# Performance work log

Hardware: AMD Instinct MI355X
Metric: run time of the kernel (lower is better)

Reference implementation:

```python
import jax, jax.numpy as jnp
import numpy as np

VS = 0.4
SENT = np.int32(2_000_000_000)  # > max lin code (1000^3)
EPS = 1e-5


def setup_inputs() -> dict:
    key = jax.random.key(0)
    ks = jax.random.split(key, 16)
    B, N, Cin, Cout = 8, 65536, 16, 128
    xyz = jax.random.uniform(ks[0], (B, N, 3), jnp.float32) * 51.2  # 128^3 voxel grid @ 0.4m
    feat = jax.random.normal(ks[1], (B, N, Cin), jnp.float32)
    mask = (jax.random.uniform(ks[2], (B, N)) < 0.9).astype(jnp.float32)
    def conv_w(k, ci, co):
        return jax.random.normal(k, (27, ci, co), jnp.float32) * (1.0 / np.sqrt(27.0 * ci))
    return {
        'xyz': xyz, 'feat': feat, 'mask': mask,
        'W1': conv_w(ks[3], Cin, 32), 'b1': jnp.zeros((32,), jnp.float32),
        'g1': jnp.ones((32,), jnp.float32), 'be1': jnp.zeros((32,), jnp.float32),
        'W2': conv_w(ks[4], 32, 64), 'b2': jnp.zeros((64,), jnp.float32),
        'g2': jnp.ones((64,), jnp.float32), 'be2': jnp.zeros((64,), jnp.float32),
        'W3': conv_w(ks[5], 64, Cout), 'b3': jnp.zeros((Cout,), jnp.float32),
        'g3': jnp.ones((Cout,), jnp.float32), 'be3': jnp.zeros((Cout,), jnp.float32),
    }


def _voxelize(lin_b, f_b, m_b):
    # sort-based unique with inverse; fixed capacity N slots (sentinel-padded)
    N = lin_b.shape[0]
    order = jnp.argsort(lin_b)
    s = lin_b[order]
    isnew = jnp.concatenate([jnp.ones((1,), bool), s[1:] != s[:-1]])
    rank = (jnp.cumsum(isnew) - 1).astype(jnp.int32)
    inv = jnp.zeros_like(lin_b).at[order].set(rank)          # point -> voxel slot
    unq = jnp.full_like(lin_b, SENT).at[rank].set(s)         # sorted unique codes, sentinel fill
    fsum = jax.ops.segment_sum(f_b * m_b[:, None], inv, num_segments=N)
    cnt = jnp.clip(jax.ops.segment_sum(m_b, inv, num_segments=N), 1.0)
    return unq, inv, fsum / cnt[:, None]


def _subm_conv(vfeat, unq, valid, W, b):
    # submanifold 3x3x3 conv on active voxels; neighbor lookup via binary search in sorted codes
    B, N, _ = vfeat.shape
    x = unq % 1000
    y = (unq // 1000) % 1000
    z = unq // 1000000
    brow = jnp.arange(B)[:, None]
    out = jnp.zeros((B, N, W.shape[-1]), vfeat.dtype)
    for ko in range(27):
        dz, dy, dx = ko // 9 - 1, (ko // 3) % 3 - 1, ko % 3 - 1
        ncode = unq + dx + 1000 * dy + 1000000 * dz
        inb = ((x + dx >= 0) & (x + dx < 1000) & (y + dy >= 0) & (y + dy < 1000)
               & (z + dz >= 0) & (z + dz < 1000))
        idx = jnp.clip(jax.vmap(jnp.searchsorted)(unq, ncode), 0, N - 1)
        found = (jnp.take_along_axis(unq, idx, 1) == ncode) & inb & valid
        nf = vfeat[brow, idx] * found[..., None].astype(vfeat.dtype)
        out = out + nf @ W[ko]
    return (out + b) * valid[..., None].astype(vfeat.dtype)


def _bn_relu(xv, g, be, valid):
    # BatchNorm1d (training stats) over valid voxel rows only, then ReLU
    w = valid[..., None].astype(xv.dtype)
    n = jnp.maximum(w.sum(), 1.0)
    mean = (xv * w).sum((0, 1)) / n
    var = (((xv - mean) ** 2) * w).sum((0, 1)) / n
    yv = (xv - mean) * jax.lax.rsqrt(var + EPS) * g + be
    return jax.nn.relu(yv) * w


def reference(xyz, feat, mask, W1, b1, g1, be1, W2, b2, g2, be2, W3, b3, g3, be3):
    B, N, _ = feat.shape
    origin = xyz.reshape(-1, 3).min(0)
    v = jnp.clip(((xyz - origin) / VS).astype(jnp.int32), 0, None)   # [B,N,3]
    lin = v[..., 0] + 1000 * (v[..., 1] + 1000 * v[..., 2])          # [B,N]
    unq, inv, vfeat = jax.vmap(_voxelize)(lin, feat, mask)
    valid = unq < SENT
    h = _bn_relu(_subm_conv(vfeat, unq, valid, W1, b1), g1, be1, valid)
    h = _bn_relu(_subm_conv(h, unq, valid, W2, b2), g2, be2, valid)
    h = _bn_relu(_subm_conv(h, unq, valid, W3, b3), g3, be3, valid)
    # scatter voxel features back to points (exact match: inv maps point -> its voxel slot)
    out_f = h[jnp.arange(B)[:, None], inv]                           # [B,N,Cout]
    return out_f * mask[..., None]
```

## Files before the change

### kernel.cpp

```cpp
#include <hip/hip_runtime.h>

#define NPTS   65536
#define NBATCH 8
#define TSIZE  131072
#define TM1    (TSIZE - 1)
#define CAP    8192
#define PPB    64
#define BMW    65536
#define STG    64
#define PCS    16

__device__ __forceinline__ unsigned hashf(int code) {
    unsigned u = (unsigned)code * 2654435761u;
    return (u >> 13) & TM1;
}

__global__ void init_origin(int* ob) {
    if (threadIdx.x < 3) ob[threadIdx.x] = 0x7F800000;
}

__global__ void minred(const float* __restrict__ xyz, int* __restrict__ ob) {
    int tid = threadIdx.x;
    float mx = INFINITY, my = INFINITY, mz = INFINITY;
    size_t total = (size_t)NBATCH * NPTS;
    for (size_t i = (size_t)blockIdx.x * blockDim.x + tid; i < total;
         i += (size_t)gridDim.x * blockDim.x) {
        mx = fminf(mx, xyz[i * 3 + 0]);
        my = fminf(my, xyz[i * 3 + 1]);
        mz = fminf(mz, xyz[i * 3 + 2]);
    }
    __shared__ float sx[256], sy[256], sz[256];
    sx[tid] = mx; sy[tid] = my; sz[tid] = mz;
    __syncthreads();
    for (int s = 128; s > 0; s >>= 1) {
        if (tid < s) {
            sx[tid] = fminf(sx[tid], sx[tid + s]);
            sy[tid] = fminf(sy[tid], sy[tid + s]);
            sz[tid] = fminf(sz[tid], sz[tid + s]);
        }
        __syncthreads();
    }
    if (tid == 0) {
        atomicMin(&ob[0], __float_as_int(sx[0]));
        atomicMin(&ob[1], __float_as_int(sy[0]));
        atomicMin(&ob[2], __float_as_int(sz[0]));
    }
}

__global__ void build_codes(const float* __restrict__ xyz, const int* __restrict__ ob,
                            int* __restrict__ pslot, int* __restrict__ hashk,
                            int* __restrict__ scnt) {
    int b = blockIdx.y;
    int p = blockIdx.x * blockDim.x + threadIdx.x;
    size_t gi = (size_t)b * NPTS + p;
    float ox = __int_as_float(ob[0]);
    float oy = __int_as_float(ob[1]);
    float oz = __int_as_float(ob[2]);
    float x = xyz[gi * 3 + 0], y = xyz[gi * 3 + 1], z = xyz[gi * 3 + 2];
    int vx = (int)((x - ox) / 0.4f); if (vx < 0) vx = 0;
    int vy = (int)((y - oy) / 0.4f); if (vy < 0) vy = 0;
    int vz = (int)((z - oz) / 0.4f); if (vz < 0) vz = 0;
    int code = vx | (vy << 7) | (vz << 14);
    int* hk = hashk + (size_t)b * TSIZE;
    unsigned s = hashf(code);
    while (true) {
        int prev = atomicCAS(&hk[s], -1, code);
        if (prev == -1 || prev == code) break;
        s = (s + 1) & TM1;
    }
    pslot[gi] = (int)s;
    atomicAdd(&scnt[(size_t)b * TSIZE + s], 1);
}

__global__ void assign_ids(const int* __restrict__ hashk, int* __restrict__ hashv,
                           int* __restrict__ nvox, int* __restrict__ voxcode,
                           unsigned* __restrict__ bitmap, const int* __restrict__ scnt,
                           int* __restrict__ vnpts) {
    int b = blockIdx.y;
    int s = blockIdx.x * blockDim.x + threadIdx.x;
    int k = hashk[(size_t)b * TSIZE + s];
    if (k != -1) {
        int id = atomicAdd(&nvox[b], 1);
        hashv[(size_t)b * TSIZE + s] = id;
        voxcode[(size_t)b * NPTS + id] = k;
        vnpts[(size_t)b * NPTS + id] = scnt[(size_t)b * TSIZE + s];
        atomicOr(&bitmap[(size_t)b * BMW + (k >> 5)], 1u << (k & 31));
    }
}

__global__ void point_pass(const int* __restrict__ pslot, const int* __restrict__ scnt,
                           const int* __restrict__ hashv, const float* __restrict__ feat,
                           const float* __restrict__ mask, int* __restrict__ inv,
                           float* __restrict__ cntf, float* __restrict__ fsum) {
    int b = blockIdx.y;
    int p = blockIdx.x * blockDim.x + threadIdx.x;
    size_t gi = (size_t)b * NPTS + p;
    int s = pslot[gi];
    int v = hashv[(size_t)b * TSIZE + s];
    inv[gi] = v;
    int n = scnt[(size_t)b * TSIZE + s];
    float m = mask[gi];
    const float4* f4 = (const float4*)(feat + gi * 16);
    float4 f0 = f4[0], f1 = f4[1], f2 = f4[2], f3 = f4[3];
    float* fs = fsum + ((size_t)b * NPTS + v) * 16;
    if (n == 1) {
        float4 o0 = {f0.x * m, f0.y * m, f0.z * m, f0.w * m};
        float4 o1 = {f1.x * m, f1.y * m, f1.z * m, f1.w * m};
        float4 o2 = {f2.x * m, f2.y * m, f2.z * m, f2.w * m};
        float4 o3 = {f3.x * m, f3.y * m, f3.z * m, f3.w * m};
        float4* fs4 = (float4*)fs;
        fs4[0] = o0; fs4[1] = o1; fs4[2] = o2; fs4[3] = o3;
    } else {
        atomicAdd(&cntf[(size_t)b * NPTS + v], m);
        atomicAdd(&fs[0],  f0.x * m); atomicAdd(&fs[1],  f0.y * m);
        atomicAdd(&fs[2],  f0.z * m); atomicAdd(&fs[3],  f0.w * m);
        atomicAdd(&fs[4],  f1.x * m); atomicAdd(&fs[5],  f1.y * m);
        atomicAdd(&fs[6],  f1.z * m); atomicAdd(&fs[7],  f1.w * m);
        atomicAdd(&fs[8],  f2.x * m); atomicAdd(&fs[9],  f2.y * m);
        atomicAdd(&fs[10], f2.z * m); atomicAdd(&fs[11], f2.w * m);
        atomicAdd(&fs[12], f3.x * m); atomicAdd(&fs[13], f3.y * m);
        atomicAdd(&fs[14], f3.z * m); atomicAdd(&fs[15], f3.w * m);
    }
}

__global__ void vfeat_div(float* __restrict__ fsum, const float* __restrict__ cntf,
                          const int* __restrict__ vnpts, const int* __restrict__ nvox) {
    int b = blockIdx.y;
    int v = blockIdx.x * blockDim.x + threadIdx.x;
    if (v >= nvox[b]) return;
    if (vnpts[(size_t)b * NPTS + v] <= 1) return;
    float cn = fmaxf(cntf[(size_t)b * NPTS + v], 1.0f);
    float* fs = fsum + ((size_t)b * NPTS + v) * 16;
    #pragma unroll
    for (int c = 0; c < 16; c++) fs[c] /= cn;
}

__global__ __launch_bounds__(256) void build_pairs(
    const int* __restrict__ hashk, const int* __restrict__ hashv,
    const int* __restrict__ voxcode, const int* __restrict__ nvox,
    const unsigned* __restrict__ bitmap,
    unsigned* __restrict__ pairs, int* __restrict__ paircnt) {
    int b = blockIdx.y;
    int t = threadIdx.x;
    int v = blockIdx.x * 256 + t;
    __shared__ int lcnt[32];
    __shared__ int lbase[32];
    __shared__ unsigned s_pay[27 * STG];
    if (t < 32) lcnt[t] = 0;
    __syncthreads();

    bool active = (v < nvox[b]);
    int code = 0;
    if (active) code = voxcode[(size_t)b * NPTS + v];
    int x = code & 127, y = (code >> 7) & 127, z = code >> 14;
    const unsigned* bm = bitmap + (size_t)b * BMW;
    const int* hk = hashk + (size_t)b * TSIZE;
    const int* hv = hashv + (size_t)b * TSIZE;

    int ncode[13];
    unsigned hitmask = 0;
    #pragma unroll
    for (int d = 0; d < 13; d++) {
        int dz = d / 9 - 1, r9 = d % 9;
        int dy = r9 / 3 - 1, dx = r9 % 3 - 1;
        int nx = x + dx, ny = y + dy, nz = z + dz;
        bool inb = active && ((unsigned)nx <= 127u) && ((unsigned)ny <= 127u) &&
                   ((unsigned)nz <= 127u);
        int nc = nx | (ny << 7) | (nz << 14);
        ncode[d] = nc;
        unsigned w = 0;
        if (inb) w = bm[nc >> 5];
        if (inb && ((w >> (nc & 31)) & 1u)) hitmask |= 1u << d;
    }

    #pragma unroll
    for (int d = 0; d < 13; d++) {
        if (hitmask & (1u << d)) {
            int nc = ncode[d];
            unsigned s = hashf(nc);
            int nb = -1;
            while (true) {
                int k = hk[s];
                if (k == nc) { nb = hv[s]; break; }
                if (k == -1) break;
                s = (s + 1) & TM1;
            }
            if (nb >= 0) {
                unsigned p1 = ((unsigned)v << 16) | (unsigned)nb;
                unsigned p2 = ((unsigned)nb << 16) | (unsigned)v;
                int l1 = atomicAdd(&lcnt[d], 1);
                if (l1 < STG) {
                    s_pay[d * STG + l1] = p1;
                } else {
                    int gs = atomicAdd(&paircnt[(b * 27 + d) * PCS], 1);
                    if (gs < CAP) pairs[(size_t)(b * 27 + d) * CAP + gs] = p1;
                }
                int k2 = 26 - d;
                int l2 = atomicAdd(&lcnt[k2], 1);
                if (l2 < STG) {
                    s_pay[k2 * STG + l2] = p2;
                } else {
                    int gs = atomicAdd(&paircnt[(b * 27 + k2) * PCS], 1);
                    if (gs < CAP) pairs[(size_t)(b * 27 + k2) * CAP + gs] = p2;
                }
            }
        }
    }
    __syncthreads();

    if (t < 27) {
        int n = lcnt[t]; if (n > STG) n = STG;
        lbase[t] = (n > 0) ? atomicAdd(&paircnt[(b * 27 + t) * PCS], n) : 0;
    }
    __syncthreads();

    for (int k = t; k < 27 * STG; k += 256) {
        int bkt = k / STG, i = k % STG;
        int n = lcnt[bkt]; if (n > STG) n = STG;
        if (i < n) {
            int gs = lbase[bkt] + i;
            if (gs < CAP) pairs[(size_t)(b * 27 + bkt) * CAP + gs] = s_pay[k];
        }
    }
}

template <int Cin, int Cout, bool XFORM>
__global__ __launch_bounds__(256) void conv_center(
    const float* __restrict__ in, float* __restrict__ outp,
    const float* __restrict__ W13, const float* __restrict__ bias,
    const float* __restrict__ sc, const float* __restrict__ sh,
    const int* __restrict__ nvox) {
    constexpr int BR  = 64;
    constexpr int CT  = (Cout < 64) ? Cout : 64;
    constexpr int RG  = 256 / CT;
    constexpr int RPT = BR / RG;
    constexpr int J   = Cout / CT;
    int b = blockIdx.y;
    int nv = nvox[b];
    int v0 = blockIdx.x * BR;
    if (v0 >= nv) return;
    __shared__ __align__(16) float A_s[Cin][BR + 4];
    __shared__ __align__(16) float W_s[Cin * Cout];
    int t = threadIdx.x;
    for (int i4 = t; i4 < Cin * Cout / 4; i4 += 256)
        ((float4*)W_s)[i4] = ((const float4*)W13)[i4];
    const float* inb = in + (size_t)b * NPTS * Cin;
    for (int i4 = t; i4 < BR * Cin / 4; i4 += 256) {
        int lin = i4 * 4;
        int r = lin / Cin, ci = lin % Cin;
        float4 val = *(const float4*)&inb[(size_t)(v0 + r) * Cin + ci];
        if (XFORM) {
            val.x = fmaxf(val.x * sc[ci + 0] + sh[ci + 0], 0.0f);
            val.y = fmaxf(val.y * sc[ci + 1] + sh[ci + 1], 0.0f);
            val.z = fmaxf(val.z * sc[ci + 2] + sh[ci + 2], 0.0f);
            val.w = fmaxf(val.w * sc[ci + 3] + sh[ci + 3], 0.0f);
        }
        A_s[ci + 0][r] = val.x;
        A_s[ci + 1][r] = val.y;
        A_s[ci + 2][r] = val.z;
        A_s[ci + 3][r] = val.w;
    }
    __syncthreads();
    int c = t % CT;
    int r0 = (t / CT) * RPT;
    float acc[RPT][J];
    #pragma unroll
    for (int r = 0; r < RPT; r++)
        #pragma unroll
        for (int j = 0; j < J; j++) acc[r][j] = 0.0f;
    #pragma unroll 4
    for (int ci = 0; ci < Cin; ci++) {
        float4 a4[RPT / 4];
        #pragma unroll
        for (int k = 0; k < RPT / 4; k++)
            a4[k] = *(const float4*)&A_s[ci][r0 + 4 * k];
        float w[J];
        #pragma unroll
        for (int j = 0; j < J; j++) w[j] = W_s[ci * Cout + c + CT * j];
        #pragma unroll
        for (int k = 0; k < RPT / 4; k++) {
            #pragma unroll
            for (int j = 0; j < J; j++) {
                acc[4 * k + 0][j] += a4[k].x * w[j];
                acc[4 * k + 1][j] += a4[k].y * w[j];
                acc[4 * k + 2][j] += a4[k].z * w[j];
                acc[4 * k + 3][j] += a4[k].w * w[j];
            }
        }
    }
    float* ob = outp + (size_t)b * NPTS * Cout;
    #pragma unroll
    for (int r = 0; r < RPT; r++) {
        int row = v0 + r0 + r;
        if (row < nv) {
            #pragma unroll
            for (int j = 0; j < J; j++)
                ob[(size_t)row * Cout + c + CT * j] = acc[r][j] + bias[c + CT * j];
        }
    }
}

template <int Cin, int Cout, bool XFORM>
__global__ __launch_bounds__(256) void conv_off(
    const float* __restrict__ in, float* __restrict__ outp,
    const float* __restrict__ W, const float* __restrict__ sc,
    const float* __restrict__ sh, const unsigned* __restrict__ pairs,
    const int* __restrict__ paircnt) {
    constexpr int BR  = PPB;
    constexpr int CT  = (Cout < 64) ? Cout : 64;
    constexpr int RG  = 256 / CT;
    constexpr int RPT = BR / RG;
    constexpr int J   = Cout / CT;
    int bk = blockIdx.y;
    int ko = bk % 27;
    int b  = bk / 27;
    int cnt = paircnt[bk * PCS];
    if (cnt > CAP) cnt = CAP;
    int start = blockIdx.x * BR;
    if (start >= cnt) return;
    int nActive = cnt - start; if (nActive > BR) nActive = BR;
    __shared__ __align__(16) float A_s[Cin][BR + 4];
    __shared__ __align__(16) float W_s[Cin * Cout];
    __shared__ unsigned pr_s[BR];
    int t = threadIdx.x;
    const float* Wk = W + (size_t)ko * Cin * Cout;
    for (int i4 = t; i4 < Cin * Cout / 4; i4 += 256)
        ((float4*)W_s)[i4] = ((const float4*)Wk)[i4];
    const unsigned* pb = pairs + (size_t)bk * CAP + start;
    if (t < BR) pr_s[t] = pb[t];
    __syncthreads();
    const float* inb = in + (size_t)b * NPTS * Cin;
    for (int i4 = t; i4 < BR * Cin / 4; i4 += 256) {
        int lin = i4 * 4;
        int r = lin / Cin, ci = lin % Cin;
        int vin = (int)(pr_s[r] & 0xffffu);
        float4 val = *(const float4*)&inb[(size_t)vin * Cin + ci];
        if (XFORM) {
            val.x = fmaxf(val.x * sc[ci + 0] + sh[ci + 0], 0.0f);
            val.y = fmaxf(val.y * sc[ci + 1] + sh[ci + 1], 0.0f);
            val.z = fmaxf(val.z * sc[ci + 2] + sh[ci + 2], 0.0f);
            val.w = fmaxf(val.w * sc[ci + 3] + sh[ci + 3], 0.0f);
        }
        A_s[ci + 0][r] = val.x;
        A_s[ci + 1][r] = val.y;
        A_s[ci + 2][r] = val.z;
        A_s[ci + 3][r] = val.w;
    }
    __syncthreads();
    int c = t % CT;
    int r0 = (t / CT) * RPT;
    float acc[RPT][J];
    #pragma unroll
    for (int r = 0; r < RPT; r++)
        #pragma unroll
        for (int j = 0; j < J; j++) acc[r][j] = 0.0f;
    #pragma unroll 4
    for (int ci = 0; ci < Cin; ci++) {
        float4 a4[RPT / 4];
        #pragma unroll
        for (int k = 0; k < RPT / 4; k++)
            a4[k] = *(const float4*)&A_s[ci][r0 + 4 * k];
        float w[J];
        #pragma unroll
        for (int j = 0; j < J; j++) w[j] = W_s[ci * Cout + c + CT * j];
        #pragma unroll
        for (int k = 0; k < RPT / 4; k++) {
            #pragma unroll
            for (int j = 0; j < J; j++) {
                acc[4 * k + 0][j] += a4[k].x * w[j];
                acc[4 * k + 1][j] += a4[k].y * w[j];
                acc[4 * k + 2][j] += a4[k].z * w[j];
                acc[4 * k + 3][j] += a4[k].w * w[j];
            }
        }
    }
    float* ob = outp + (size_t)b * NPTS * Cout;
    #pragma unroll
    for (int r = 0; r < RPT; r++) {
        if (r0 + r < nActive) {
            int vout = (int)(pr_s[r0 + r] >> 16);
            #pragma unroll
            for (int j = 0; j < J; j++)
                atomicAdd(&ob[(size_t)vout * Cout + c + CT * j], acc[r][j]);
        }
    }
}

template <int C>
__global__ void bn_stats(const float* __restrict__ h, const int* __restrict__ nvox,
                         float* __restrict__ sums) {
    constexpr int RPB = 256 / C;
    int b = blockIdx.y;
    int nv = nvox[b];
    int tid = threadIdx.x;
    int c = tid % C;
    int r = tid / C;
    float s0 = 0.0f, s1 = 0.0f;
    for (int v = blockIdx.x * RPB + r; v < nv; v += gridDim.x * RPB) {
        float x = h[((size_t)b * NPTS + v) * C + c];
        s0 += x;
        s1 += x * x;
    }
    __shared__ float l0[256], l1[256];
    l0[tid] = s0; l1[tid] = s1;
    __syncthreads();
    for (int s = 128; s >= C; s >>= 1) {
        if (tid < s) { l0[tid] += l0[tid + s]; l1[tid] += l1[tid + s]; }
        __syncthreads();
    }
    if (tid < C) {
        atomicAdd(&sums[c], l0[tid]);
        atomicAdd(&sums[C + c], l1[tid]);
    }
}

template <int C>
__global__ void bn_finalize(const float* __restrict__ sums, const int* __restrict__ nvox,
                            const float* __restrict__ g, const float* __restrict__ be,
                            float* __restrict__ scale, float* __restrict__ shift) {
    int c = threadIdx.x;
    if (c >= C) return;
    float n = 0.0f;
    for (int b = 0; b < NBATCH; b++) n += (float)nvox[b];
    n = fmaxf(n, 1.0f);
    float mean = sums[c] / n;
    float var = sums[C + c] / n - mean * mean;
    float a = g[c] * rsqrtf(var + 1e-5f);
    scale[c] = a;
    shift[c] = be[c] - mean * a;
}

__global__ void out_gather(const float* __restrict__ h3, const int* __restrict__ inv,
                           const float* __restrict__ mask, const float* __restrict__ sc,
                           const float* __restrict__ sh, float* __restrict__ out) {
    int b = blockIdx.y;
    size_t i = (size_t)blockIdx.x * blockDim.x + threadIdx.x;
    int p = (int)(i >> 7);
    int c = (int)(i & 127);
    size_t gi = (size_t)b * NPTS + p;
    int v = inv[gi];
    float m = mask[gi];
    float x = h3[((size_t)b * NPTS + v) * 128 + c];
    x = fmaxf(x * sc[c] + sh[c], 0.0f);
    out[gi * 128 + c] = x * m;
}

extern "C" void kernel_launch(void* const* d_in, const int* in_sizes, int n_in,
                              void* d_out, int out_size, void* d_ws, size_t ws_size,
                              hipStream_t stream) {
    const float* xyz  = (const float*)d_in[0];
    const float* feat = (const float*)d_in[1];
    const float* mask = (const float*)d_in[2];
    const float* W1 = (const float*)d_in[3];
    const float* b1 = (const float*)d_in[4];
    const float* g1 = (const float*)d_in[5];
    const float* be1 = (const float*)d_in[6];
    const float* W2 = (const float*)d_in[7];
    const float* b2 = (const float*)d_in[8];
    const float* g2 = (const float*)d_in[9];
    const float* be2 = (const float*)d_in[10];
    const float* W3 = (const float*)d_in[11];
    const float* b3 = (const float*)d_in[12];
    const float* g3 = (const float*)d_in[13];
    const float* be3 = (const float*)d_in[14];
    float* out = (float*)d_out;

    char* ws = (char*)d_ws;
    size_t off = 0;
    auto alloc = [&](size_t bytes) {
        void* p = ws + off;
        off += (bytes + 255) & ~(size_t)255;
        return p;
    };
    int*      hashk   = (int*)alloc((size_t)NBATCH * TSIZE * 4);
    int*      hashv   = (int*)alloc((size_t)NBATCH * TSIZE * 4);
    int*      scnt    = (int*)alloc((size_t)NBATCH * TSIZE * 4);
    int*      nvox    = (int*)alloc(NBATCH * 4);
    int*      origin  = (int*)alloc(16);
    int*      pslot   = (int*)alloc((size_t)NBATCH * NPTS * 4);
    int*      voxcode = (int*)alloc((size_t)NBATCH * NPTS * 4);
    int*      vnpts   = (int*)alloc((size_t)NBATCH * NPTS * 4);
    int*      inv     = (int*)alloc((size_t)NBATCH * NPTS * 4);
    float*    cntf    = (float*)alloc((size_t)NBATCH * NPTS * 4);
    unsigned* pairs   = (unsigned*)alloc((size_t)NBATCH * 27 * CAP * 4);
    int*      paircnt = (int*)alloc((size_t)NBATCH * 27 * PCS * 4);
    unsigned* bitmap  = (unsigned*)alloc((size_t)NBATCH * BMW * 4);
    float*    bnsums  = (float*)alloc(256 * 4);
    float*    bnscale = (float*)alloc(128 * 4);
    float*    bnshift = (float*)alloc(128 * 4);
    float*    A       = (float*)alloc((size_t)NBATCH * NPTS * 64 * 4);
    float*    Bb      = (float*)alloc((size_t)NBATCH * NPTS * 128 * 4);

    hipMemsetAsync(hashk, 0xFF, (size_t)NBATCH * TSIZE * 4, stream);
    hipMemsetAsync(scnt, 0, (size_t)NBATCH * TSIZE * 4, stream);
    hipMemsetAsync(nvox, 0, NBATCH * 4, stream);
    hipMemsetAsync(cntf, 0, (size_t)NBATCH * NPTS * 4, stream);
    hipMemsetAsync(A, 0, (size_t)NBATCH * NPTS * 16 * 4, stream);
    hipMemsetAsync(paircnt, 0, (size_t)NBATCH * 27 * PCS * 4, stream);
    hipMemsetAsync(bitmap, 0, (size_t)NBATCH * BMW * 4, stream);
    init_origin<<<1, 64, 0, stream>>>(origin);

    minred<<<512, 256, 0, stream>>>(xyz, origin);
    build_codes<<<dim3(NPTS / 256, NBATCH), 256, 0, stream>>>(xyz, origin, pslot, hashk, scnt);
    assign_ids<<<dim3(TSIZE / 256, NBATCH), 256, 0, stream>>>(hashk, hashv, nvox, voxcode,
                                                              bitmap, scnt, vnpts);
    point_pass<<<dim3(NPTS / 256, NBATCH), 256, 0, stream>>>(pslot, scnt, hashv, feat, mask,
                                                             inv, cntf, A);
    vfeat_div<<<dim3(NPTS / 256, NBATCH), 256, 0, stream>>>(A, cntf, vnpts, nvox);

    build_pairs<<<dim3(NPTS / 256, NBATCH), 256, 0, stream>>>(hashk, hashv, voxcode,
                                                              nvox, bitmap, pairs, paircnt);

    dim3 cgrid(NPTS / 64, NBATCH);
    dim3 ogrid(CAP / PPB, NBATCH * 27);

    conv_center<16, 32, false><<<cgrid, 256, 0, stream>>>(A, Bb, W1 + 13 * 16 * 32, b1,
                                                          nullptr, nullptr, nvox);
    conv_off<16, 32, false><<<ogrid, 256, 0, stream>>>(A, Bb, W1, nullptr, nullptr,
                                                       pairs, paircnt);
    hipMemsetAsync(bnsums, 0, 256 * 4, stream);
    bn_stats<32><<<dim3(64, NBATCH), 256, 0, stream>>>(Bb, nvox, bnsums);
    bn_finalize<32><<<1, 128, 0, stream>>>(bnsums, nvox, g1, be1, bnscale, bnshift);

    conv_center<32, 64, true><<<cgrid, 256, 0, stream>>>(Bb, A, W2 + 13 * 32 * 64, b2,
                                                         bnscale, bnshift, nvox);
    conv_off<32, 64, true><<<ogrid, 256, 0, stream>>>(Bb, A, W2, bnscale, bnshift,
                                                      pairs, paircnt);
    hipMemsetAsync(bnsums, 0, 256 * 4, stream);
    bn_stats<64><<<dim3(64, NBATCH), 256, 0, stream>>>(A, nvox, bnsums);
    bn_finalize<64><<<1, 128, 0, stream>>>(bnsums, nvox, g2, be2, bnscale, bnshift);

    conv_center<64, 128, true><<<cgrid, 256, 0, stream>>>(A, Bb, W3 + 13 * 64 * 128, b3,
                                                          bnscale, bnshift, nvox);
    conv_off<64, 128, true><<<ogrid, 256, 0, stream>>>(A, Bb, W3, bnscale, bnshift,
                                                       pairs, paircnt);
    hipMemsetAsync(bnsums, 0, 256 * 4, stream);
    bn_stats<128><<<dim3(64, NBATCH), 256, 0, stream>>>(Bb, nvox, bnsums);
    bn_finalize<128><<<1, 128, 0, stream>>>(bnsums, nvox, g3, be3, bnscale, bnshift);

    out_gather<<<dim3(NPTS * 128 / 256, NBATCH), 256, 0, stream>>>(Bb, inv, mask, bnscale,
                                                                   bnshift, out);
}
```

Baseline: 1.759 ms.

## Aggregate voxel id atomics, drop shared weight staging, swizzle LDS, vectorize gather

```diff
diff --git a/kernel.cpp b/kernel.cpp
--- a/kernel.cpp
+++ b/kernel.cpp
@@ -79,8 +79,22 @@
     int b = blockIdx.y;
     int s = blockIdx.x * blockDim.x + threadIdx.x;
     int k = hashk[(size_t)b * TSIZE + s];
+    unsigned long long vote = __ballot(k != -1);
+    __shared__ int wbase[4];
+    int wid = threadIdx.x >> 6, lane = threadIdx.x & 63;
+    if (lane == 0) wbase[wid] = __popcll(vote);
+    __syncthreads();
+    if (threadIdx.x == 0) {
+        int c0 = wbase[0], c1 = wbase[1], c2 = wbase[2], c3 = wbase[3];
+        int base = atomicAdd(&nvox[b], c0 + c1 + c2 + c3);
+        wbase[0] = base;
+        wbase[1] = base + c0;
+        wbase[2] = base + c0 + c1;
+        wbase[3] = base + c0 + c1 + c2;
+    }
+    __syncthreads();
     if (k != -1) {
-        int id = atomicAdd(&nvox[b], 1);
+        int id = wbase[wid] + __popcll(vote & ((1ull << lane) - 1ull));
         hashv[(size_t)b * TSIZE + s] = id;
         voxcode[(size_t)b * NPTS + id] = k;
         vnpts[(size_t)b * NPTS + id] = scnt[(size_t)b * TSIZE + s];
@@ -225,7 +239,7 @@
 }
 
 template <int Cin, int Cout, bool XFORM>
-__global__ __launch_bounds__(256) void conv_center(
+__global__ __launch_bounds__(256, 4) void conv_center(
     const float* __restrict__ in, float* __restrict__ outp,
     const float* __restrict__ W13, const float* __restrict__ bias,
     const float* __restrict__ sc, const float* __restrict__ sh,
@@ -240,10 +254,7 @@
     int v0 = blockIdx.x * BR;
     if (v0 >= nv) return;
     __shared__ __align__(16) float A_s[Cin][BR + 4];
-    __shared__ __align__(16) float W_s[Cin * Cout];
     int t = threadIdx.x;
-    for (int i4 = t; i4 < Cin * Cout / 4; i4 += 256)
-        ((float4*)W_s)[i4] = ((const float4*)W13)[i4];
     const float* inb = in + (size_t)b * NPTS * Cin;
     for (int i4 = t; i4 < BR * Cin / 4; i4 += 256) {
         int lin = i4 * 4;
@@ -255,10 +266,10 @@
             val.z = fmaxf(val.z * sc[ci + 2] + sh[ci + 2], 0.0f);
             val.w = fmaxf(val.w * sc[ci + 3] + sh[ci + 3], 0.0f);
         }
-        A_s[ci + 0][r] = val.x;
-        A_s[ci + 1][r] = val.y;
-        A_s[ci + 2][r] = val.z;
-        A_s[ci + 3][r] = val.w;
+        A_s[ci + 0][r ^ ((ci + 0) & 28)] = val.x;
+        A_s[ci + 1][r ^ ((ci + 1) & 28)] = val.y;
+        A_s[ci + 2][r ^ ((ci + 2) & 28)] = val.z;
+        A_s[ci + 3][r ^ ((ci + 3) & 28)] = val.w;
     }
     __syncthreads();
     int c = t % CT;
@@ -270,38 +281,39 @@
         for (int j = 0; j < J; j++) acc[r][j] = 0.0f;
     #pragma unroll 4
     for (int ci = 0; ci < Cin; ci++) {
-        float4 a4[RPT / 4];
-        #pragma unroll
-        for (int k = 0; k < RPT / 4; k++)
-            a4[k] = *(const float4*)&A_s[ci][r0 + 4 * k];
+        int sw = ci & 28;
         float w[J];
         #pragma unroll
-        for (int j = 0; j < J; j++) w[j] = W_s[ci * Cout + c + CT * j];
+        for (int j = 0; j < J; j++) w[j] = W13[(size_t)ci * Cout + c + CT * j];
         #pragma unroll
         for (int k = 0; k < RPT / 4; k++) {
+            float4 a4 = *(const float4*)&A_s[ci][(r0 + 4 * k) ^ sw];
             #pragma unroll
             for (int j = 0; j < J; j++) {
-                acc[4 * k + 0][j] += a4[k].x * w[j];
-                acc[4 * k + 1][j] += a4[k].y * w[j];
-                acc[4 * k + 2][j] += a4[k].z * w[j];
-                acc[4 * k + 3][j] += a4[k].w * w[j];
+                acc[4 * k + 0][j] += a4.x * w[j];
+                acc[4 * k + 1][j] += a4.y * w[j];
+                acc[4 * k + 2][j] += a4.z * w[j];
+                acc[4 * k + 3][j] += a4.w * w[j];
             }
         }
     }
     float* ob = outp + (size_t)b * NPTS * Cout;
+    float bs[J];
+    #pragma unroll
+    for (int j = 0; j < J; j++) bs[j] = bias[c + CT * j];
     #pragma unroll
     for (int r = 0; r < RPT; r++) {
         int row = v0 + r0 + r;
         if (row < nv) {
             #pragma unroll
             for (int j = 0; j < J; j++)
-                ob[(size_t)row * Cout + c + CT * j] = acc[r][j] + bias[c + CT * j];
+                ob[(size_t)row * Cout + c + CT * j] = acc[r][j] + bs[j];
         }
     }
 }
 
 template <int Cin, int Cout, bool XFORM>
-__global__ __launch_bounds__(256) void conv_off(
+__global__ __launch_bounds__(256, 4) void conv_off(
     const float* __restrict__ in, float* __restrict__ outp,
     const float* __restrict__ W, const float* __restrict__ sc,
     const float* __restrict__ sh, const unsigned* __restrict__ pairs,
@@ -320,12 +332,9 @@
     if (start >= cnt) return;
     int nActive = cnt - start; if (nActive > BR) nActive = BR;
     __shared__ __align__(16) float A_s[Cin][BR + 4];
-    __shared__ __align__(16) float W_s[Cin * Cout];
     __shared__ unsigned pr_s[BR];
     int t = threadIdx.x;
     const float* Wk = W + (size_t)ko * Cin * Cout;
-    for (int i4 = t; i4 < Cin * Cout / 4; i4 += 256)
-        ((float4*)W_s)[i4] = ((const float4*)Wk)[i4];
     const unsigned* pb = pairs + (size_t)bk * CAP + start;
     if (t < BR) pr_s[t] = pb[t];
     __syncthreads();
@@ -341,10 +350,10 @@
             val.z = fmaxf(val.z * sc[ci + 2] + sh[ci + 2], 0.0f);
             val.w = fmaxf(val.w * sc[ci + 3] + sh[ci + 3], 0.0f);
         }
-        A_s[ci + 0][r] = val.x;
-        A_s[ci + 1][r] = val.y;
-        A_s[ci + 2][r] = val.z;
-        A_s[ci + 3][r] = val.w;
+        A_s[ci + 0][r ^ ((ci + 0) & 28)] = val.x;
+        A_s[ci + 1][r ^ ((ci + 1) & 28)] = val.y;
+        A_s[ci + 2][r ^ ((ci + 2) & 28)] = val.z;
+        A_s[ci + 3][r ^ ((ci + 3) & 28)] = val.w;
     }
     __syncthreads();
     int c = t % CT;
@@ -356,21 +365,19 @@
         for (int j = 0; j < J; j++) acc[r][j] = 0.0f;
     #pragma unroll 4
     for (int ci = 0; ci < Cin; ci++) {
-        float4 a4[RPT / 4];
-        #pragma unroll
-        for (int k = 0; k < RPT / 4; k++)
-            a4[k] = *(const float4*)&A_s[ci][r0 + 4 * k];
+        int sw = ci & 28;
         float w[J];
         #pragma unroll
-        for (int j = 0; j < J; j++) w[j] = W_s[ci * Cout + c + CT * j];
+        for (int j = 0; j < J; j++) w[j] = Wk[(size_t)ci * Cout + c + CT * j];
         #pragma unroll
         for (int k = 0; k < RPT / 4; k++) {
+            float4 a4 = *(const float4*)&A_s[ci][(r0 + 4 * k) ^ sw];
             #pragma unroll
             for (int j = 0; j < J; j++) {
-                acc[4 * k + 0][j] += a4[k].x * w[j];
-                acc[4 * k + 1][j] += a4[k].y * w[j];
-                acc[4 * k + 2][j] += a4[k].z * w[j];
-                acc[4 * k + 3][j] += a4[k].w * w[j];
+                acc[4 * k + 0][j] += a4.x * w[j];
+                acc[4 * k + 1][j] += a4.y * w[j];
+                acc[4 * k + 2][j] += a4.z * w[j];
+                acc[4 * k + 3][j] += a4.w * w[j];
             }
         }
     }
@@ -434,15 +441,21 @@
                            const float* __restrict__ mask, const float* __restrict__ sc,
                            const float* __restrict__ sh, float* __restrict__ out) {
     int b = blockIdx.y;
-    size_t i = (size_t)blockIdx.x * blockDim.x + threadIdx.x;
-    int p = (int)(i >> 7);
-    int c = (int)(i & 127);
+    int i = blockIdx.x * blockDim.x + threadIdx.x;
+    int p = i >> 5;
+    int c4 = (i & 31) * 4;
     size_t gi = (size_t)b * NPTS + p;
     int v = inv[gi];
     float m = mask[gi];
-    float x = h3[((size_t)b * NPTS + v) * 128 + c];
-    x = fmaxf(x * sc[c] + sh[c], 0.0f);
-    out[gi * 128 + c] = x * m;
+    float4 x = *(const float4*)&h3[((size_t)b * NPTS + v) * 128 + c4];
+    float4 s = *(const float4*)&sc[c4];
+    float4 h = *(const float4*)&sh[c4];
+    float4 o;
+    o.x = fmaxf(x.x * s.x + h.x, 0.0f) * m;
+    o.y = fmaxf(x.y * s.y + h.y, 0.0f) * m;
+    o.z = fmaxf(x.z * s.z + h.z, 0.0f) * m;
+    o.w = fmaxf(x.w * s.w + h.w, 0.0f) * m;
+    *(float4*)&out[gi * 128 + c4] = o;
 }
 
 extern "C" void kernel_launch(void* const* d_in, const int* in_sizes, int n_in,
@@ -538,6 +551,6 @@
     bn_stats<128><<<dim3(64, NBATCH), 256, 0, stream>>>(Bb, nvox, bnsums);
     bn_finalize<128><<<1, 128, 0, stream>>>(bnsums, nvox, g3, be3, bnscale, bnshift);
 
-    out_gather<<<dim3(NPTS * 128 / 256, NBATCH), 256, 0, stream>>>(Bb, inv, mask, bnscale,
-                                                                   bnshift, out);
-}
+    out_gather<<<dim3(NPTS * 32 / 256, NBATCH), 256, 0, stream>>>(Bb, inv, mask, bnscale,
+                                                                  bnshift, out);
+}
```

Measured after the change: 1.446 ms. -17.8%, faster.
